# Kernel optimization log

Measured on AMD Instinct MI355X. Metric: run time of the kernel, lower is better.

The kernel has to match this reference:

```python
import jax, jax.numpy as jnp
import numpy as np

TAU = 0.5          # proto_tau
TOPK = 3           # slot_topk
BETA = 0.5         # soft-topk temperature
BETA_SUP = 0.4     # support_beta
T_SUP = 1.6        # support_tsup
KAPPA_FEAT = 1.0   # support_kappa_feat
CMAX = 64          # num classes


def setup_inputs() -> dict:
    key = jax.random.key(0)
    k0, k1, k2, k3 = jax.random.split(key, 4)
    B, M, D, K = 128, 64, 512, 4096
    feats_bmd = jax.random.normal(k0, (B, M, D), jnp.float32)
    slot_prob = jax.random.uniform(k1, (B, M), jnp.float32)
    slot_mask = jnp.ones((M,), jnp.float32)
    S_slots = jax.random.normal(k2, (B, M, D), jnp.float32)
    C = jax.random.normal(k3, (K, D), jnp.float32)
    # every class gets K//CMAX prototypes (torch.unique loop covers all classes)
    C_cls = jnp.arange(K, dtype=jnp.int32) % CMAX
    alpha = jnp.array(1.0, jnp.float32)
    return dict(feats_bmd=feats_bmd, slot_prob=slot_prob, slot_mask=slot_mask,
                S_slots=S_slots, C=C, C_cls=C_cls, alpha=alpha)


def _l2norm(x, eps=1e-12):
    return x / jnp.maximum(jnp.linalg.norm(x, axis=-1, keepdims=True), eps)


def _soft_topk_weights(p, mask, k=TOPK, beta=BETA):
    # p: (B,M), mask: (1,M)
    p = p * mask
    _, topi = jax.lax.top_k(p, k)                          # (B,k)
    keep = jnp.zeros_like(p).at[jnp.arange(p.shape[0])[:, None], topi].set(1.0)
    q = p * keep
    z = (q - q.mean(axis=1, keepdims=True)) / beta
    w = jax.nn.softmax(z, axis=1) * mask
    return w / jnp.maximum(w.sum(axis=1, keepdims=True), 1e-8)


def _class_lse(sim, cls, num_classes, tau=TAU):
    # segmented logsumexp over prototypes grouped by class id (replaces the
    # per-class masked_fill loop in the original).
    B, M, K = sim.shape
    s = sim.reshape(B * M, K).T                                   # (K, BM)
    xmax = jax.ops.segment_max(s, cls, num_segments=num_classes)  # (C, BM)
    e = jnp.exp((s - xmax[cls]) / tau)
    ssum = jax.ops.segment_sum(e, cls, num_segments=num_classes)  # (C, BM)
    evi = xmax + tau * jnp.log(jnp.maximum(ssum, 1e-8))
    return evi.T.reshape(B, M, num_classes)


def _top1_plus_support(evi, P, S_slots):
    # evi: (B,M,C), P: (B,M), S_slots: (B,M,D)
    B, M, C = evi.shape
    score = evi * P[:, :, None]
    top1_idx = jnp.argmax(score, axis=1)                    # (B,C)
    top1_val = jnp.max(score, axis=1)                       # (B,C)
    P_sup = jax.nn.softmax(jnp.log(P + 1e-8) / T_SUP, axis=1)  # (B,M)
    S = _l2norm(S_slots)
    top1_feat = jnp.take_along_axis(S, top1_idx[:, :, None], axis=1)  # (B,C,D)
    cos = jnp.maximum(jnp.einsum('bmd,bcd->bmc', S, top1_feat), 0.0)
    w_red = KAPPA_FEAT * cos
    support_raw = evi + jnp.log(jnp.maximum(P_sup, 1e-8))[:, :, None] - w_red
    is_top1 = jnp.arange(M)[None, :, None] == top1_idx[:, None, :]    # (B,M,C)
    support_raw = jnp.where(is_top1, -10000.0, support_raw)
    support_val = jax.nn.logsumexp(support_raw, axis=1)
    return top1_val + BETA_SUP * support_val


def reference(feats_bmd, slot_prob, slot_mask, S_slots, C, C_cls, alpha):
    w = _soft_topk_weights(slot_prob, slot_mask[None, :])
    f = _l2norm(feats_bmd)
    sim = jnp.einsum('bmd,kd->bmk', f, C)        # (B,M,K) similarity GEMM
    evi_all = _class_lse(sim, C_cls, CMAX)       # (B,M,Cmax)
    proto_logits = _top1_plus_support(evi_all, w, S_slots)
    return alpha * proto_logits                  # (B, Cmax)
```

## Files before the change

### kernel.cpp

```cpp
#include <hip/hip_runtime.h>
#include <stdint.h>


typedef short   short8_t  __attribute__((ext_vector_type(8)));
typedef unsigned short ushort8_t __attribute__((ext_vector_type(8)));
typedef float   floatx4   __attribute__((ext_vector_type(4)));

#define B_N   128
#define M_N   64
#define D_N   512
#define K_N   4096
#define ROWS  8192

__device__ __forceinline__ unsigned short f2bf(float f){
  unsigned u = __float_as_uint(f);
  u = (u + 0x7FFFu + ((u >> 16) & 1u)) >> 16;
  return (unsigned short)u;
}
__device__ __forceinline__ float bf2f(unsigned short s){
  return __uint_as_float(((unsigned)s) << 16);
}

__global__ __launch_bounds__(256) void k_prep(
    const float* __restrict__ feats, const float* __restrict__ Cm,
    unsigned short* __restrict__ fhi, unsigned short* __restrict__ flo,
    unsigned short* __restrict__ chi, unsigned short* __restrict__ clo){
  const int bid = blockIdx.x;
  const bool isF = bid < 2048;
  const int lane = threadIdx.x & 63;
  const int row  = (isF ? bid : bid - 2048) * 4 + (threadIdx.x >> 6);
  const float* src = isF ? feats : Cm;
  const float4* r = (const float4*)(src + (size_t)row * D_N);
  float4 a = r[lane*2], c = r[lane*2 + 1];
  float inv = 1.f;
  if(isF){
    float ss = a.x*a.x + a.y*a.y + a.z*a.z + a.w*a.w
             + c.x*c.x + c.y*c.y + c.z*c.z + c.w*c.w;
    #pragma unroll
    for(int off = 32; off > 0; off >>= 1) ss += __shfl_xor(ss, off);
    inv = 1.f / fmaxf(sqrtf(ss), 1e-12f);
  }
  float v[8] = {a.x*inv, a.y*inv, a.z*inv, a.w*inv, c.x*inv, c.y*inv, c.z*inv, c.w*inv};
  ushort8_t h, L;
  #pragma unroll
  for(int i = 0; i < 8; ++i){
    h[i] = f2bf(v[i]);
    L[i] = f2bf(v[i] - bf2f(h[i]));
  }
  unsigned short* hi = isF ? fhi : chi;
  unsigned short* lo = isF ? flo : clo;
  ((ushort8_t*)(hi + (size_t)row * D_N))[lane] = h;
  ((ushort8_t*)(lo + (size_t)row * D_N))[lane] = L;
}

__device__ __forceinline__ floatx4 mfma16(short8_t a, short8_t b, floatx4 c){
  return __builtin_amdgcn_mfma_f32_16x16x32_bf16(a, b, c, 0, 0, 0);
}

__global__ __launch_bounds__(512, 4) void k_gemm_lse(
    const unsigned short* __restrict__ fhi, const unsigned short* __restrict__ flo,
    const unsigned short* __restrict__ chi, const unsigned short* __restrict__ clo,
    float* __restrict__ part){
  __shared__ char smem[81920];
  const int bid = blockIdx.x;
  const int kq  = bid & 3;
  const int rg  = bid >> 2;
  const int tid = threadIdx.x;
  const int w = tid >> 6, lane = tid & 63;
  const int wr = w >> 2, wc = w & 3;
  const int l15 = lane & 15, l4 = lane >> 4, ax = l15 & 7;

  const int srow = tid >> 3, ss = tid & 7;
  const int aoff = srow*128 + ((ss ^ (srow & 7)) << 4);
  const char* aH = (const char*)fhi + (size_t)(rg*64 + srow)*1024 + ss*16;
  const char* aL = (const char*)flo + (size_t)(rg*64 + srow)*1024 + ss*16;
  const char* bH = (const char*)chi + (size_t)(kq*1024 + srow)*1024 + ss*16;
  const char* bL = (const char*)clo + (size_t)(kq*1024 + srow)*1024 + ss*16;

  const int arB = (32*wr + l15) * 128;
  const int brB = (wc*16 + l15) * 128;

  const floatx4 vzero = {0.f, 0.f, 0.f, 0.f};
  floatx4 cacc[2];
  cacc[0] = vzero; cacc[1] = vzero;
  floatx4 sim[2][4];
  #pragma unroll
  for(int rt = 0; rt < 2; ++rt)
    #pragma unroll
    for(int kt = 0; kt < 4; ++kt) sim[rt][kt] = vzero;

  short8_t pre[10];
  {
    pre[0] = *(const short8_t*)(aH);
    pre[1] = *(const short8_t*)(aL);
    #pragma unroll
    for(int kt = 0; kt < 4; ++kt) pre[2+kt] = *(const short8_t*)(bH + kt*65536);
    #pragma unroll
    for(int kt = 0; kt < 4; ++kt) pre[6+kt] = *(const short8_t*)(bL + kt*65536);
    *(short8_t*)(smem + aoff)         = pre[0];
    *(short8_t*)(smem + 8192  + aoff) = pre[1];
    #pragma unroll
    for(int kt = 0; kt < 4; ++kt) *(short8_t*)(smem + 16384 + kt*8192 + aoff) = pre[2+kt];
    #pragma unroll
    for(int kt = 0; kt < 4; ++kt) *(short8_t*)(smem + 49152 + kt*8192 + aoff) = pre[6+kt];
  }
  __syncthreads();

  #pragma unroll 1
  for(int s = 0; s < 32; ++s){
    const int dc = s & 7;
    if(s < 31){
      const int sn = s + 1;
      const int koff = (sn >> 3) * 262144;
      const int doff = (sn & 7) * 128;
      pre[0] = *(const short8_t*)(aH + doff);
      pre[1] = *(const short8_t*)(aL + doff);
      #pragma unroll
      for(int kt = 0; kt < 4; ++kt)
        pre[2+kt] = *(const short8_t*)(bH + koff + kt*65536 + doff);
      #pragma unroll
      for(int kt = 0; kt < 4; ++kt)
        pre[6+kt] = *(const short8_t*)(bL + koff + kt*65536 + doff);
    }

    __builtin_amdgcn_s_setprio(1);
    #pragma unroll
    for(int ks = 0; ks < 2; ++ks){
      const int sx = ((ks*4 + l4) ^ ax) << 4;
      short8_t ah0 = *(const short8_t*)(smem + arB + sx);
      short8_t ah1 = *(const short8_t*)(smem + arB + 2048 + sx);
      short8_t al0 = *(const short8_t*)(smem + 8192 + arB + sx);
      short8_t al1 = *(const short8_t*)(smem + 8192 + arB + 2048 + sx);
      #pragma unroll
      for(int kt = 0; kt < 4; ++kt){
        short8_t bh = *(const short8_t*)(smem + 16384 + kt*8192 + brB + sx);
        short8_t bl = *(const short8_t*)(smem + 49152 + kt*8192 + brB + sx);
        sim[0][kt] = mfma16(ah0, bh, sim[0][kt]);
        sim[0][kt] = mfma16(al0, bh, sim[0][kt]);
        sim[0][kt] = mfma16(ah0, bl, sim[0][kt]);
        sim[1][kt] = mfma16(ah1, bh, sim[1][kt]);
        sim[1][kt] = mfma16(al1, bh, sim[1][kt]);
        sim[1][kt] = mfma16(ah1, bl, sim[1][kt]);
      }
    }
    __builtin_amdgcn_s_setprio(0);

    if(dc == 7){
      #pragma unroll
      for(int rt = 0; rt < 2; ++rt)
        #pragma unroll
        for(int kt = 0; kt < 4; ++kt){
          #pragma unroll
          for(int e = 0; e < 4; ++e)
            cacc[rt][e] += __expf(2.0f * sim[rt][kt][e]);
          sim[rt][kt] = vzero;
        }
    }

    __syncthreads();
    if(s < 31){
      *(short8_t*)(smem + aoff)         = pre[0];
      *(short8_t*)(smem + 8192  + aoff) = pre[1];
      #pragma unroll
      for(int kt = 0; kt < 4; ++kt) *(short8_t*)(smem + 16384 + kt*8192 + aoff) = pre[2+kt];
      #pragma unroll
      for(int kt = 0; kt < 4; ++kt) *(short8_t*)(smem + 49152 + kt*8192 + aoff) = pre[6+kt];
      __syncthreads();
    }
  }

  #pragma unroll
  for(int rt = 0; rt < 2; ++rt)
    #pragma unroll
    for(int e = 0; e < 4; ++e){
      const int r = 32*wr + 16*rt + l4*4 + e;
      part[((size_t)kq*ROWS + rg*64 + r)*64 + wc*16 + l15] = cacc[rt][e];
    }
}

#define SPAD 516
__global__ __launch_bounds__(256) void k_epi(
    const float* __restrict__ part, const float* __restrict__ S_raw,
    const float* __restrict__ prob, const float* __restrict__ maskp,
    const float* __restrict__ alpha_p, float* __restrict__ out){
  __shared__ float Ss[64 * SPAD];
  __shared__ float evi[64 * 64];
  __shared__ float w_s[64], lps_s[64], t1v[64];
  __shared__ int   t1i[64];
  __shared__ float red[16 * 64];
  const int b = blockIdx.x, tid = threadIdx.x;

  if(tid < 64){
    const int m = tid;
    const float mk = maskp[m];
    float p = prob[b*M_N + m] * mk;
    float pw = p, keep = 0.f;
    for(int it = 0; it < 3; ++it){
      float v = pw; int idx = m;
      #pragma unroll
      for(int off = 32; off > 0; off >>= 1){
        float ov = __shfl_xor(v, off);
        int   oi = __shfl_xor(idx, off);
        if(ov > v || (ov == v && oi < idx)){ v = ov; idx = oi; }
      }
      if(m == idx){ keep = 1.f; pw = -1e30f; }
    }
    float q = p * keep;
    float s = q;
    #pragma unroll
    for(int off = 32; off > 0; off >>= 1) s += __shfl_xor(s, off);
    float z = (q - s * (1.f/64.f)) * 2.0f;
    float zm = z;
    #pragma unroll
    for(int off = 32; off > 0; off >>= 1) zm = fmaxf(zm, __shfl_xor(zm, off));
    float e = expf(z - zm);
    float es = e;
    #pragma unroll
    for(int off = 32; off > 0; off >>= 1) es += __shfl_xor(es, off);
    float wv = (e / es) * mk;
    float ws = wv;
    #pragma unroll
    for(int off = 32; off > 0; off >>= 1) ws += __shfl_xor(ws, off);
    wv = wv / fmaxf(ws, 1e-8f);
    w_s[m] = wv;
    float l = logf(wv + 1e-8f) * (1.0f/1.6f);
    float lm = l;
    #pragma unroll
    for(int off = 32; off > 0; off >>= 1) lm = fmaxf(lm, __shfl_xor(lm, off));
    float ee = expf(l - lm);
    float ees = ee;
    #pragma unroll
    for(int off = 32; off > 0; off >>= 1) ees += __shfl_xor(ees, off);
    lps_s[m] = logf(fmaxf(ee / ees, 1e-8f));
  }

  for(int i = tid; i < 4096; i += 256){
    float s = part[(size_t)b*4096 + i]
            + part[(size_t)1*ROWS*64 + (size_t)b*4096 + i]
            + part[(size_t)2*ROWS*64 + (size_t)b*4096 + i]
            + part[(size_t)3*ROWS*64 + (size_t)b*4096 + i];
    evi[i] = 0.5f * logf(s);
  }
  const float4* sg = (const float4*)(S_raw + (size_t)b * 32768);
  for(int i = tid; i < 8192; i += 256){
    int r = i >> 7, c4 = i & 127;
    *(float4*)&Ss[r*SPAD + c4*4] = sg[i];
  }
  __syncthreads();

  {
    const int lane = tid & 63;
    for(int it = 0; it < 16; ++it){
      const int row = it*4 + (tid >> 6);
      float4 x = *(const float4*)&Ss[row*SPAD + lane*8];
      float4 y = *(const float4*)&Ss[row*SPAD + lane*8 + 4];
      float ss = x.x*x.x + x.y*x.y + x.z*x.z + x.w*x.w
               + y.x*y.x + y.y*y.y + y.z*y.z + y.w*y.w;
      #pragma unroll
      for(int off = 32; off > 0; off >>= 1) ss += __shfl_xor(ss, off);
      float inv = 1.f / fmaxf(sqrtf(ss), 1e-12f);
      x.x*=inv; x.y*=inv; x.z*=inv; x.w*=inv;
      y.x*=inv; y.y*=inv; y.z*=inv; y.w*=inv;
      *(float4*)&Ss[row*SPAD + lane*8]     = x;
      *(float4*)&Ss[row*SPAD + lane*8 + 4] = y;
    }
  }
  __syncthreads();

  if(tid < 64){
    float bv = -1e30f; int bi = 0;
    for(int m = 0; m < 64; ++m){
      float sc = evi[m*64 + tid] * w_s[m];
      if(sc > bv){ bv = sc; bi = m; }
    }
    t1v[tid] = bv; t1i[tid] = bi;
  }
  __syncthreads();

  const int mi = tid >> 4, ci = tid & 15;
  float acc[4][4];
  #pragma unroll
  for(int i = 0; i < 4; ++i)
    #pragma unroll
    for(int j = 0; j < 4; ++j) acc[i][j] = 0.f;
  int tr[4];
  #pragma unroll
  for(int q = 0; q < 4; ++q) tr[q] = t1i[ci*4 + q];

  for(int d4 = 0; d4 < 128; ++d4){
    float4 sv[4], tv[4];
    #pragma unroll
    for(int q = 0; q < 4; ++q) sv[q] = *(const float4*)&Ss[(mi*4 + q)*SPAD + d4*4];
    #pragma unroll
    for(int q = 0; q < 4; ++q) tv[q] = *(const float4*)&Ss[tr[q]*SPAD + d4*4];
    #pragma unroll
    for(int i = 0; i < 4; ++i)
      #pragma unroll
      for(int j = 0; j < 4; ++j)
        acc[i][j] += sv[i].x*tv[j].x + sv[i].y*tv[j].y + sv[i].z*tv[j].z + sv[i].w*tv[j].w;
  }

  float ps[4] = {0.f, 0.f, 0.f, 0.f};
  #pragma unroll
  for(int i = 0; i < 4; ++i){
    const int m = mi*4 + i;
    #pragma unroll
    for(int q = 0; q < 4; ++q){
      const int c = ci*4 + q;
      float sr = evi[m*64 + c] + lps_s[m] - fmaxf(acc[i][q], 0.f);
      ps[q] += (m == tr[q]) ? 0.f : expf(sr);
    }
  }
  #pragma unroll
  for(int q = 0; q < 4; ++q) red[mi*64 + ci*4 + q] = ps[q];
  __syncthreads();

  if(tid < 64){
    float s = 0.f;
    for(int i = 0; i < 16; ++i) s += red[i*64 + tid];
    out[b*64 + tid] = alpha_p[0] * (t1v[tid] + 0.4f * logf(s));
  }
}

extern "C" void kernel_launch(void* const* d_in, const int* in_sizes, int n_in,
                              void* d_out, int out_size, void* d_ws, size_t ws_size,
                              hipStream_t stream){
  const float* feats     = (const float*)d_in[0];
  const float* slot_prob = (const float*)d_in[1];
  const float* slot_mask = (const float*)d_in[2];
  const float* S_slots   = (const float*)d_in[3];
  const float* Cmat      = (const float*)d_in[4];
  const float* alpha     = (const float*)d_in[6];

  char* ws = (char*)d_ws;
  unsigned short* fhi = (unsigned short*)(ws);
  unsigned short* flo = (unsigned short*)(ws + (8  << 20));
  unsigned short* chi = (unsigned short*)(ws + (16 << 20));
  unsigned short* clo = (unsigned short*)(ws + (20 << 20));
  float* part  = (float*)(ws + (24 << 20));
  float* outp  = (float*)d_out;

  k_prep<<<dim3(3072), dim3(256), 0, stream>>>(feats, Cmat, fhi, flo, chi, clo);
  k_gemm_lse<<<dim3(512), dim3(512), 0, stream>>>(fhi, flo, chi, clo, part);
  k_epi<<<dim3(128), dim3(256), 0, stream>>>(part, S_slots, slot_prob, slot_mask,
                                             alpha, outp);
}
```

Before: 225.4 us.

## Retile similarity GEMM to 128x512 blocks with double-buffered LDS and intra-block class reduction

The fused GEMM+exp kernel now gives each block 128 rows and 512 prototypes (8 prototype groups instead of 4), with each wave holding a 4x4 grid of MFMA tiles over 32-wide D chunks. It double-buffers the staged tiles in LDS so only one barrier per step is needed, and it reduces the per-class exp sums across the four column waves through LDS before writing partials. The goal is more register-level reuse of A and B fragments and less synchronisation. The cost is higher register pressure (launch bounds drop to 2 blocks per CU), dropping the XOR swizzle, which may bring LDS bank conflicts, and twice as many partial buffers for the epilogue to sum.

```diff
diff --git a/kernel.cpp b/kernel.cpp
--- a/kernel.cpp
+++ b/kernel.cpp
@@ -57,125 +57,146 @@
   return __builtin_amdgcn_mfma_f32_16x16x32_bf16(a, b, c, 0, 0, 0);
 }
 
-__global__ __launch_bounds__(512, 4) void k_gemm_lse(
+__global__ __launch_bounds__(512, 2) void k_gemm_lse(
     const unsigned short* __restrict__ fhi, const unsigned short* __restrict__ flo,
     const unsigned short* __restrict__ chi, const unsigned short* __restrict__ clo,
     float* __restrict__ part){
-  __shared__ char smem[81920];
+  __shared__ char smem[98304];
   const int bid = blockIdx.x;
-  const int kq  = bid & 3;
-  const int rg  = bid >> 2;
+  const int pg  = bid & 7;
+  const int rg  = bid >> 3;
   const int tid = threadIdx.x;
   const int w = tid >> 6, lane = tid & 63;
   const int wr = w >> 2, wc = w & 3;
-  const int l15 = lane & 15, l4 = lane >> 4, ax = l15 & 7;
-
-  const int srow = tid >> 3, ss = tid & 7;
-  const int aoff = srow*128 + ((ss ^ (srow & 7)) << 4);
-  const char* aH = (const char*)fhi + (size_t)(rg*64 + srow)*1024 + ss*16;
-  const char* aL = (const char*)flo + (size_t)(rg*64 + srow)*1024 + ss*16;
-  const char* bH = (const char*)chi + (size_t)(kq*1024 + srow)*1024 + ss*16;
-  const char* bL = (const char*)clo + (size_t)(kq*1024 + srow)*1024 + ss*16;
-
-  const int arB = (32*wr + l15) * 128;
-  const int brB = (wc*16 + l15) * 128;
-
-  const floatx4 vzero = {0.f, 0.f, 0.f, 0.f};
-  floatx4 cacc[2];
-  cacc[0] = vzero; cacc[1] = vzero;
-  floatx4 sim[2][4];
-  #pragma unroll
-  for(int rt = 0; rt < 2; ++rt)
-    #pragma unroll
-    for(int kt = 0; kt < 4; ++kt) sim[rt][kt] = vzero;
-
-  short8_t pre[10];
+  const int l15 = lane & 15, l4 = lane >> 4;
+
+  const int arow = tid >> 2, aslot = tid & 3;
+  const char* aH = (const char*)fhi + ((size_t)(rg*128 + arow))*1024 + aslot*16;
+  const char* aL = (const char*)flo + ((size_t)(rg*128 + arow))*1024 + aslot*16;
+  const char* bH = (const char*)chi + ((size_t)(pg*512 + arow))*1024 + aslot*16;
+  const char* bL = (const char*)clo + ((size_t)(pg*512 + arow))*1024 + aslot*16;
+  const int ldst = tid * 16;
+
+  const int fro = l15*64 + l4*16;
+  const int aBase = wr*4096;
+  const int bBase = 16384 + wc*4096;
+
+  floatx4 sim[4][4];
+  float  cacc[4][4][4];
+  #pragma unroll
+  for(int rf = 0; rf < 4; ++rf)
+    #pragma unroll
+    for(int cf = 0; cf < 4; ++cf){
+      sim[rf][cf] = (floatx4){0.f,0.f,0.f,0.f};
+      #pragma unroll
+      for(int e = 0; e < 4; ++e) cacc[rf][cf][e] = 0.f;
+    }
+
+  short8_t p0, p1, p2, p3, p4, p5;
+  p0 = *(const short8_t*)(aH);
+  p1 = *(const short8_t*)(aL);
+  p2 = *(const short8_t*)(bH);
+  p3 = *(const short8_t*)(bH + 131072);
+  p4 = *(const short8_t*)(bL);
+  p5 = *(const short8_t*)(bL + 131072);
   {
-    pre[0] = *(const short8_t*)(aH);
-    pre[1] = *(const short8_t*)(aL);
-    #pragma unroll
-    for(int kt = 0; kt < 4; ++kt) pre[2+kt] = *(const short8_t*)(bH + kt*65536);
-    #pragma unroll
-    for(int kt = 0; kt < 4; ++kt) pre[6+kt] = *(const short8_t*)(bL + kt*65536);
-    *(short8_t*)(smem + aoff)         = pre[0];
-    *(short8_t*)(smem + 8192  + aoff) = pre[1];
-    #pragma unroll
-    for(int kt = 0; kt < 4; ++kt) *(short8_t*)(smem + 16384 + kt*8192 + aoff) = pre[2+kt];
-    #pragma unroll
-    for(int kt = 0; kt < 4; ++kt) *(short8_t*)(smem + 49152 + kt*8192 + aoff) = pre[6+kt];
-  }
-  __syncthreads();
+    char* buf = smem;
+    *(short8_t*)(buf + ldst)                 = p0;
+    *(short8_t*)(buf + 8192  + ldst)         = p1;
+    *(short8_t*)(buf + 16384 + ldst)         = p2;
+    *(short8_t*)(buf + 16384 + 8192 + ldst)  = p3;
+    *(short8_t*)(buf + 32768 + ldst)         = p4;
+    *(short8_t*)(buf + 32768 + 8192 + ldst)  = p5;
+  }
 
   #pragma unroll 1
   for(int s = 0; s < 32; ++s){
-    const int dc = s & 7;
     if(s < 31){
       const int sn = s + 1;
-      const int koff = (sn >> 3) * 262144;
-      const int doff = (sn & 7) * 128;
-      pre[0] = *(const short8_t*)(aH + doff);
-      pre[1] = *(const short8_t*)(aL + doff);
-      #pragma unroll
-      for(int kt = 0; kt < 4; ++kt)
-        pre[2+kt] = *(const short8_t*)(bH + koff + kt*65536 + doff);
-      #pragma unroll
-      for(int kt = 0; kt < 4; ++kt)
-        pre[6+kt] = *(const short8_t*)(bL + koff + kt*65536 + doff);
-    }
+      const int da = (sn & 15) * 64;
+      const size_t db = (size_t)(sn >> 4) * 262144 + da;
+      p0 = *(const short8_t*)(aH + da);
+      p1 = *(const short8_t*)(aL + da);
+      p2 = *(const short8_t*)(bH + db);
+      p3 = *(const short8_t*)(bH + 131072 + db);
+      p4 = *(const short8_t*)(bL + db);
+      p5 = *(const short8_t*)(bL + 131072 + db);
+    }
+
+    __syncthreads();
+    char* buf = smem + (s & 1) * 49152;
 
     __builtin_amdgcn_s_setprio(1);
-    #pragma unroll
-    for(int ks = 0; ks < 2; ++ks){
-      const int sx = ((ks*4 + l4) ^ ax) << 4;
-      short8_t ah0 = *(const short8_t*)(smem + arB + sx);
-      short8_t ah1 = *(const short8_t*)(smem + arB + 2048 + sx);
-      short8_t al0 = *(const short8_t*)(smem + 8192 + arB + sx);
-      short8_t al1 = *(const short8_t*)(smem + 8192 + arB + 2048 + sx);
-      #pragma unroll
-      for(int kt = 0; kt < 4; ++kt){
-        short8_t bh = *(const short8_t*)(smem + 16384 + kt*8192 + brB + sx);
-        short8_t bl = *(const short8_t*)(smem + 49152 + kt*8192 + brB + sx);
-        sim[0][kt] = mfma16(ah0, bh, sim[0][kt]);
-        sim[0][kt] = mfma16(al0, bh, sim[0][kt]);
-        sim[0][kt] = mfma16(ah0, bl, sim[0][kt]);
-        sim[1][kt] = mfma16(ah1, bh, sim[1][kt]);
-        sim[1][kt] = mfma16(al1, bh, sim[1][kt]);
-        sim[1][kt] = mfma16(ah1, bl, sim[1][kt]);
+    short8_t ah[4], al[4];
+    #pragma unroll
+    for(int rf = 0; rf < 4; ++rf){
+      ah[rf] = *(const short8_t*)(buf + aBase + rf*1024 + fro);
+      al[rf] = *(const short8_t*)(buf + 8192 + aBase + rf*1024 + fro);
+    }
+    #pragma unroll
+    for(int cf = 0; cf < 4; ++cf){
+      short8_t bh = *(const short8_t*)(buf + bBase + cf*1024 + fro);
+      short8_t bl = *(const short8_t*)(buf + 16384 + bBase + cf*1024 + fro);
+      #pragma unroll
+      for(int rf = 0; rf < 4; ++rf){
+        sim[rf][cf] = mfma16(ah[rf], bh, sim[rf][cf]);
+        sim[rf][cf] = mfma16(al[rf], bh, sim[rf][cf]);
+        sim[rf][cf] = mfma16(ah[rf], bl, sim[rf][cf]);
       }
     }
     __builtin_amdgcn_s_setprio(0);
 
-    if(dc == 7){
-      #pragma unroll
-      for(int rt = 0; rt < 2; ++rt)
+    if(s < 31){
+      char* nb = smem + ((s + 1) & 1) * 49152;
+      *(short8_t*)(nb + ldst)                 = p0;
+      *(short8_t*)(nb + 8192  + ldst)         = p1;
+      *(short8_t*)(nb + 16384 + ldst)         = p2;
+      *(short8_t*)(nb + 16384 + 8192 + ldst)  = p3;
+      *(short8_t*)(nb + 32768 + ldst)         = p4;
+      *(short8_t*)(nb + 32768 + 8192 + ldst)  = p5;
+    }
+
+    if((s & 15) == 15){
+      #pragma unroll
+      for(int rf = 0; rf < 4; ++rf)
         #pragma unroll
-        for(int kt = 0; kt < 4; ++kt){
+        for(int cf = 0; cf < 4; ++cf){
           #pragma unroll
           for(int e = 0; e < 4; ++e)
-            cacc[rt][e] += __expf(2.0f * sim[rt][kt][e]);
-          sim[rt][kt] = vzero;
+            cacc[rf][cf][e] += __expf(2.0f * sim[rf][cf][e]);
+          sim[rf][cf] = (floatx4){0.f,0.f,0.f,0.f};
         }
     }
-
-    __syncthreads();
-    if(s < 31){
-      *(short8_t*)(smem + aoff)         = pre[0];
-      *(short8_t*)(smem + 8192  + aoff) = pre[1];
-      #pragma unroll
-      for(int kt = 0; kt < 4; ++kt) *(short8_t*)(smem + 16384 + kt*8192 + aoff) = pre[2+kt];
-      #pragma unroll
-      for(int kt = 0; kt < 4; ++kt) *(short8_t*)(smem + 49152 + kt*8192 + aoff) = pre[6+kt];
-      __syncthreads();
-    }
-  }
-
-  #pragma unroll
-  for(int rt = 0; rt < 2; ++rt)
-    #pragma unroll
-    for(int e = 0; e < 4; ++e){
-      const int r = 32*wr + 16*rt + l4*4 + e;
-      part[((size_t)kq*ROWS + rg*64 + r)*64 + wc*16 + l15] = cacc[rt][e];
-    }
+  }
+
+  __syncthreads();
+  if(wc > 0){
+    float* sl = (float*)(smem + (wr*3 + wc - 1) * 16384);
+    #pragma unroll
+    for(int rf = 0; rf < 4; ++rf)
+      #pragma unroll
+      for(int cf = 0; cf < 4; ++cf)
+        #pragma unroll
+        for(int e = 0; e < 4; ++e)
+          sl[(rf*16 + l4*4 + e)*64 + cf*16 + l15] = cacc[rf][cf][e];
+  }
+  __syncthreads();
+  if(wc == 0){
+    const float* s0 = (const float*)(smem + (wr*3 + 0) * 16384);
+    const float* s1 = (const float*)(smem + (wr*3 + 1) * 16384);
+    const float* s2 = (const float*)(smem + (wr*3 + 2) * 16384);
+    #pragma unroll
+    for(int rf = 0; rf < 4; ++rf)
+      #pragma unroll
+      for(int cf = 0; cf < 4; ++cf)
+        #pragma unroll
+        for(int e = 0; e < 4; ++e){
+          const int idx = (rf*16 + l4*4 + e)*64 + cf*16 + l15;
+          const float v = cacc[rf][cf][e] + s0[idx] + s1[idx] + s2[idx];
+          const int row = rg*128 + wr*64 + rf*16 + l4*4 + e;
+          part[((size_t)pg*ROWS + row)*64 + cf*16 + l15] = v;
+        }
+  }
 }
 
 #define SPAD 516
@@ -235,10 +256,10 @@
   }
 
   for(int i = tid; i < 4096; i += 256){
-    float s = part[(size_t)b*4096 + i]
-            + part[(size_t)1*ROWS*64 + (size_t)b*4096 + i]
-            + part[(size_t)2*ROWS*64 + (size_t)b*4096 + i]
-            + part[(size_t)3*ROWS*64 + (size_t)b*4096 + i];
+    float s = 0.f;
+    #pragma unroll
+    for(int pg = 0; pg < 8; ++pg)
+      s += part[(size_t)pg*ROWS*64 + (size_t)b*4096 + i];
     evi[i] = 0.5f * logf(s);
   }
   const float4* sg = (const float4*)(S_raw + (size_t)b * 32768);
```

After: 230.7 us. +2.3%, slower.
